# Optimization experiments

Measured on AMD Instinct MI355X. Metric: run time of the kernel, lower is better.

The kernel has to match this reference:

```python
import jax, jax.numpy as jnp
import numpy as np
jax.config.update("jax_enable_x64", True)  # int64 needed for the prime-product duplicate hash

EPSILON = 1e-6
SIGMA_BOOST = 2.0
B, N, CHUNK, R = 16, 4096, 32, 2
K = N // CHUNK            # 128 chunks
GADD, RADD = 8, 8
NPOINTS = 2 ** R + GADD + RADD   # 20 integer tuples per mean
L = CHUNK * NPOINTS              # 640 tuples per chunk
OUT, IN = 1024, 1024
RNG = np.array([OUT, IN], dtype=np.float32)      # subrange for the learned cols (out dim, in dim)
REGION = np.array([8.0, 8.0], dtype=np.float32)  # relative sampling range
# itertools.product([True, False], repeat=2) -> floor/ceil selection mask
FLOOR_MASK = jnp.array([[True, True], [True, False], [False, True], [False, False]])


def setup_inputs() -> dict:
    key = jax.random.key(0)
    ks = jax.random.split(key, 6)
    return {
        "input": jax.random.normal(ks[0], (B, IN), jnp.float32),
        "res": jax.random.normal(ks[1], (B, N, R + 2), jnp.float32),   # raw hypernetwork output
        "bias": jax.random.normal(ks[2], (OUT,), jnp.float32),          # dense bias (Bias.DENSE)
        "u_global": jax.random.uniform(ks[3], (B, K, CHUNK, GADD, R), jnp.float32),
        "u_rel": jax.random.uniform(ks[4], (B, K, CHUNK, RADD, R), jnp.float32),
        "temp_indices": jax.random.randint(ks[5], (N, 2), 0, OUT, jnp.int64),
    }


def reference(input, res, bias, u_global, u_rel, temp_indices):
    rngv = jnp.asarray(RNG)    # (R,) sizes of learned dims
    rrng = jnp.asarray(REGION)

    # ---- split_out: activations on raw hypernetwork output ----
    means = jax.nn.sigmoid(res[:, :, :R]) * (rngv - 1.0)                                  # (B,N,R)
    sigmas = (jax.nn.softplus(res[:, :, R] + SIGMA_BOOST) + EPSILON)[:, :, None] * rngv   # (B,N,R)
    values = res[:, :, R + 1]                                                             # (B,N)

    means = means.reshape(B, K, CHUNK, R)
    sigmas = sigmas.reshape(B, K, CHUNK, R)
    values = values.reshape(B, K, CHUNK)

    # ---- generate_integer_tuples (non-differentiable: uses means.data) ----
    m = jax.lax.stop_gradient(means)
    mexp = m[:, :, :, None, :]                                       # (B,K,C,1,R)
    neighbor = jnp.where(FLOOR_MASK[None, None, None], jnp.floor(mexp), jnp.ceil(mexp))  # (B,K,C,4,R)
    sampled = jnp.floor(u_global * (1.0 - EPSILON) * rngv)           # (B,K,C,GADD,R)
    mns = jnp.round(m)[:, :, :, None, :]
    lower = mns - rrng * 0.5
    upper = mns + rrng * 0.5
    lower = jnp.where(lower < 0.0, 0.0, lower)
    lower = jnp.where(upper > rngv, rngv - rrng, lower)
    rr = jnp.floor(u_rel * (1.0 - EPSILON) * rrng + lower)           # (B,K,C,RADD,R)
    ints = jnp.concatenate([neighbor, sampled, rr], axis=3)          # (B,K,C,NPOINTS,R)
    ints = ints.reshape(B, K, L, R).astype(jnp.int64)

    # ---- duplicates: prime-product hash, sort, compare neighbors, unsort ----
    primes = jnp.array([2, 3], jnp.int64)[:R]
    h = jnp.prod((ints + 1) ** primes, axis=-1)                      # (B,K,L) int64
    sidx = jnp.argsort(h, axis=2)
    hs = jnp.take_along_axis(h, sidx, 2)
    dmask = jnp.concatenate([jnp.zeros((B, K, 1), bool), hs[:, :, 1:] == hs[:, :, :-1]], axis=2)
    dups = jnp.take_along_axis(dmask, jnp.argsort(sidx, axis=2), 2)  # (B,K,L)

    # ---- densities: sum_r (p-m)^2/(eps+sigma), via quadratic expansion (avoids 5D tensor) ----
    pts = ints.astype(jnp.float32)                                   # (B,K,L,R)
    isig = 1.0 / (EPSILON + sigmas)                                  # (B,K,C,R)
    t1 = jnp.einsum('bklr,bkcr->bklc', pts * pts, isig)
    t2 = jnp.einsum('bklr,bkcr->bklc', pts, isig * means)
    t3 = jnp.sum(isig * means * means, axis=-1)                      # (B,K,C)
    props = jnp.exp(-0.5 * (t1 - 2.0 * t2 + t3[:, :, None, :]))      # (B,K,L,C)

    # zero duplicates, normalize over tuples, distribute values
    props = props * (~dups)[:, :, :, None].astype(jnp.float32)
    props = props / jnp.sum(props, axis=2, keepdims=True)
    vals = jnp.sum(props * values[:, :, None, :], axis=3)            # (B,K,L)

    # ---- stitch learned columns into the hardwired template ----
    flat_idx = ints.reshape(B, K * L, R)
    template = jnp.broadcast_to(temp_indices[None, :, None, :], (B, N, NPOINTS, 2)).reshape(B, K * L, 2)
    full_idx = template.at[:, :, jnp.array([0, 1])].set(flat_idx)    # learn_cols = (0, 1)
    out_idx = full_idx[:, :, 0]                                      # index into out_size
    in_idx = full_idx[:, :, 1]                                       # index into input dim
    vflat = vals.reshape(B, K * L)

    # ---- sparse matrix * input: gather, weight, scatter-add ----
    gathered = vflat * jnp.take_along_axis(input, in_idx, axis=1)    # (B, K*L)
    flat = (jnp.arange(B)[:, None] * OUT + out_idx).reshape(-1)
    y = jnp.zeros((B * OUT,), jnp.float32).at[flat].add(gathered.reshape(-1)).reshape(B, OUT)
    return y + bias[None, :]
```

## Files before the change

### kernel.cpp

```cpp
#include <hip/hip_runtime.h>
#include <hip/hip_fp16.h>
#include <math.h>

#define NBATCH 16
#define CH     32
#define NP     20
#define LPTS   640
#define DIMO   1024
#define TAB    2048

__global__ void init_out_kernel(const float* __restrict__ bias, float* __restrict__ out) {
    int i = blockIdx.x * blockDim.x + threadIdx.x;
    if (i < NBATCH * DIMO) out[i] = bias[i & (DIMO - 1)];
}

__device__ __forceinline__ float wave_sum63(float v) {
    v += __int_as_float(__builtin_amdgcn_update_dpp(0, __float_as_int(v), 0x111, 0xF, 0xF, true));
    v += __int_as_float(__builtin_amdgcn_update_dpp(0, __float_as_int(v), 0x112, 0xF, 0xF, true));
    v += __int_as_float(__builtin_amdgcn_update_dpp(0, __float_as_int(v), 0x114, 0xF, 0xF, true));
    v += __int_as_float(__builtin_amdgcn_update_dpp(0, __float_as_int(v), 0x118, 0xF, 0xF, true));
    v += __int_as_float(__builtin_amdgcn_update_dpp(0, __float_as_int(v), 0x142, 0xA, 0xF, true));
    v += __int_as_float(__builtin_amdgcn_update_dpp(0, __float_as_int(v), 0x143, 0xC, 0xF, true));
    return v;
}

__global__ __launch_bounds__(LPTS, 8) void hyper_kernel(
    const float* __restrict__ input,
    const float* __restrict__ res,
    const float* __restrict__ u_global,
    const float* __restrict__ u_rel,
    float* __restrict__ out)
{
    __shared__ float4 cpar[CH];
    __shared__ float cm0[CH], cm1[CH], cval[CH], colsum[CH];
    __shared__ __align__(16) float cscale[CH];
    __shared__ unsigned long long keys[TAB];
    __shared__ int mins[TAB];
    __shared__ float outacc[DIMO];

    const int bk  = blockIdx.x;
    const int b   = bk >> 7;
    const int tid = threadIdx.x;

    #pragma unroll
    for (int i = tid; i < TAB; i += LPTS) { keys[i] = 0ULL; mins[i] = 0x7fffffff; }
    outacc[tid] = 0.0f;
    if (tid < DIMO - LPTS) outacc[tid + LPTS] = 0.0f;

    if (tid < CH) {
        colsum[tid] = 0.0f;
        const float* rp = res + (size_t)(bk * CH + tid) * 4;
        const float r0 = rp[0], r1 = rp[1], r2 = rp[2], r3 = rp[3];
        const float m0 = (1.0f / (1.0f + expf(-r0))) * 1023.0f;
        const float m1 = (1.0f / (1.0f + expf(-r1))) * 1023.0f;
        const float xx = r2 + 2.0f;
        const float sp = fmaxf(xx, 0.0f) + log1pf(expf(-fabsf(xx)));
        const float sig = (sp + 1e-6f) * 1024.0f;
        const float isig = 1.0f / (1e-6f + sig);
        cm0[tid] = m0; cm1[tid] = m1;
        cpar[tid] = make_float4(isig, isig * m0, isig * m1, isig * (m0 * m0 + m1 * m1));
        cval[tid] = r3;
    }
    __syncthreads();

    const int c = tid / NP;
    const int p = tid - c * NP;
    const float m0 = cm0[c], m1 = cm1[c];
    const float CEPS = (float)(1.0 - 1e-6);

    int x, y;
    if (p < 4) {
        x = (int)((p & 2) ? ceilf(m0) : floorf(m0));
        y = (int)((p & 1) ? ceilf(m1) : floorf(m1));
    } else if (p < 12) {
        const float* up = u_global + (size_t)(((bk * CH + c) * 8 + (p - 4)) * 2);
        x = (int)floorf((up[0] * CEPS) * 1024.0f);
        y = (int)floorf((up[1] * CEPS) * 1024.0f);
    } else {
        const float* up = u_rel + (size_t)(((bk * CH + c) * 8 + (p - 12)) * 2);
        const float mn0 = rintf(m0), mn1 = rintf(m1);
        float lo0 = mn0 - 4.0f; if (lo0 < 0.0f) lo0 = 0.0f; if (mn0 + 4.0f > 1024.0f) lo0 = 1016.0f;
        float lo1 = mn1 - 4.0f; if (lo1 < 0.0f) lo1 = 0.0f; if (mn1 + 4.0f > 1024.0f) lo1 = 1016.0f;
        x = (int)floorf((up[0] * CEPS) * 8.0f + lo0);
        y = (int)floorf((up[1] * CEPS) * 8.0f + lo1);
    }

    const long long xi = (long long)x + 1;
    const long long yi = (long long)y + 1;
    const unsigned long long h = (unsigned long long)(xi * xi * (yi * yi * yi));

    unsigned int hh = (unsigned int)(h ^ (h >> 31));
    hh *= 2654435761u;
    int idx = (int)(hh >> 21);
    for (;;) {
        unsigned long long prev = atomicCAS(&keys[idx], 0ULL, h);
        if (prev == 0ULL || prev == h) break;
        idx = (idx + 1) & (TAB - 1);
    }
    atomicMin(&mins[idx], tid);
    __syncthreads();
    const float keep = (mins[idx] == tid) ? 1.0f : 0.0f;

    const float px = (float)x, py = (float)y;
    const float p2 = px * px + py * py;
    const bool lane63 = (tid & 63) == 63;

    __half2 pc[CH / 2];
    #pragma unroll
    for (int j = 0; j < CH / 2; ++j) {
        const float4 cp0 = cpar[2 * j];
        const float4 cp1 = cpar[2 * j + 1];
        const float d0 = cp0.x * p2 - 2.0f * (px * cp0.y + py * cp0.z) + cp0.w;
        const float d1 = cp1.x * p2 - 2.0f * (px * cp1.y + py * cp1.z) + cp1.w;
        const float v0 = __expf(-0.5f * d0) * keep;
        const float v1 = __expf(-0.5f * d1) * keep;
        pc[j] = __floats2half2_rn(v0, v1);
        const float s0 = wave_sum63(v0);
        const float s1 = wave_sum63(v1);
        if (lane63) {
            atomicAdd(&colsum[2 * j], s0);
            atomicAdd(&colsum[2 * j + 1], s1);
        }
    }
    __syncthreads();
    if (tid < CH) cscale[tid] = cval[tid] / colsum[tid];
    __syncthreads();

    float val = 0.0f;
    const float4* cs4 = reinterpret_cast<const float4*>(cscale);
    #pragma unroll
    for (int i = 0; i < CH / 4; ++i) {
        const float4 sc = cs4[i];
        const float2 f0 = __half22float2(pc[2 * i]);
        const float2 f1 = __half22float2(pc[2 * i + 1]);
        val += f0.x * sc.x + f0.y * sc.y + f1.x * sc.z + f1.y * sc.w;
    }

    const float g = val * input[b * DIMO + y];
    atomicAdd(&outacc[x], g);
    __syncthreads();

    {
        const float v0 = outacc[tid];
        if (v0 != 0.0f) atomicAdd(&out[b * DIMO + tid], v0);
        if (tid < DIMO - LPTS) {
            const float v1 = outacc[tid + LPTS];
            if (v1 != 0.0f) atomicAdd(&out[b * DIMO + tid + LPTS], v1);
        }
    }
}

extern "C" void kernel_launch(void* const* d_in, const int* in_sizes, int n_in,
                              void* d_out, int out_size, void* d_ws, size_t ws_size,
                              hipStream_t stream) {
    const float* input  = (const float*)d_in[0];
    const float* res    = (const float*)d_in[1];
    const float* bias   = (const float*)d_in[2];
    const float* u_glob = (const float*)d_in[3];
    const float* u_rel  = (const float*)d_in[4];
    float* out = (float*)d_out;

    hipLaunchKernelGGL(init_out_kernel, dim3((NBATCH * DIMO + 255) / 256), dim3(256), 0, stream,
                       bias, out);
    hipLaunchKernelGGL(hyper_kernel, dim3(NBATCH * 128), dim3(LPTS), 0, stream,
                       input, res, u_glob, u_rel, out);
}
```

Baseline: 125.0 us.

## Process two tuples per thread, alias output accumulator onto hash table, fold bias

Halves the block size to 320 threads, each handling two tuples (chunks c and c+16), so the wave reductions for column sums cover two values at once. The shared outacc buffer reuses the hash-key storage after dedup, which cuts LDS use per block. The init kernel is replaced by a memset, with bias added by the kk==0 block of each batch. Hashing now uses 32-bit products and float2 loads. More registers per thread may limit occupancy.

```diff
diff --git a/kernel.cpp b/kernel.cpp
--- a/kernel.cpp
+++ b/kernel.cpp
@@ -6,13 +6,9 @@
 #define CH     32
 #define NP     20
 #define LPTS   640
+#define NT     320
 #define DIMO   1024
 #define TAB    2048
-
-__global__ void init_out_kernel(const float* __restrict__ bias, float* __restrict__ out) {
-    int i = blockIdx.x * blockDim.x + threadIdx.x;
-    if (i < NBATCH * DIMO) out[i] = bias[i & (DIMO - 1)];
-}
 
 __device__ __forceinline__ float wave_sum63(float v) {
     v += __int_as_float(__builtin_amdgcn_update_dpp(0, __float_as_int(v), 0x111, 0xF, 0xF, true));
@@ -24,9 +20,10 @@
     return v;
 }
 
-__global__ __launch_bounds__(LPTS, 8) void hyper_kernel(
+__global__ __launch_bounds__(NT, 8) void hyper_kernel(
     const float* __restrict__ input,
     const float* __restrict__ res,
+    const float* __restrict__ bias,
     const float* __restrict__ u_global,
     const float* __restrict__ u_rel,
     float* __restrict__ out)
@@ -36,16 +33,17 @@
     __shared__ __align__(16) float cscale[CH];
     __shared__ unsigned long long keys[TAB];
     __shared__ int mins[TAB];
-    __shared__ float outacc[DIMO];
+    float* const outacc = reinterpret_cast<float*>(keys);
 
     const int bk  = blockIdx.x;
     const int b   = bk >> 7;
+    const int kk  = bk & 127;
     const int tid = threadIdx.x;
+    const int c0  = tid / NP;
+    const int p   = tid - c0 * NP;
+    const int c1  = c0 + 16;
 
-    #pragma unroll
-    for (int i = tid; i < TAB; i += LPTS) { keys[i] = 0ULL; mins[i] = 0x7fffffff; }
-    outacc[tid] = 0.0f;
-    if (tid < DIMO - LPTS) outacc[tid + LPTS] = 0.0f;
+    for (int i = tid; i < TAB; i += NT) { keys[i] = 0ULL; mins[i] = 0x7fffffff; }
 
     if (tid < CH) {
         colsum[tid] = 0.0f;
@@ -63,90 +61,119 @@
     }
     __syncthreads();
 
-    const int c = tid / NP;
-    const int p = tid - c * NP;
-    const float m0 = cm0[c], m1 = cm1[c];
     const float CEPS = (float)(1.0 - 1e-6);
-
-    int x, y;
-    if (p < 4) {
-        x = (int)((p & 2) ? ceilf(m0) : floorf(m0));
-        y = (int)((p & 1) ? ceilf(m1) : floorf(m1));
-    } else if (p < 12) {
-        const float* up = u_global + (size_t)(((bk * CH + c) * 8 + (p - 4)) * 2);
-        x = (int)floorf((up[0] * CEPS) * 1024.0f);
-        y = (int)floorf((up[1] * CEPS) * 1024.0f);
-    } else {
-        const float* up = u_rel + (size_t)(((bk * CH + c) * 8 + (p - 12)) * 2);
-        const float mn0 = rintf(m0), mn1 = rintf(m1);
-        float lo0 = mn0 - 4.0f; if (lo0 < 0.0f) lo0 = 0.0f; if (mn0 + 4.0f > 1024.0f) lo0 = 1016.0f;
-        float lo1 = mn1 - 4.0f; if (lo1 < 0.0f) lo1 = 0.0f; if (mn1 + 4.0f > 1024.0f) lo1 = 1016.0f;
-        x = (int)floorf((up[0] * CEPS) * 8.0f + lo0);
-        y = (int)floorf((up[1] * CEPS) * 8.0f + lo1);
+    int x0, y0, x1, y1;
+    {
+        const float2* ug = reinterpret_cast<const float2*>(u_global);
+        const float2* ur = reinterpret_cast<const float2*>(u_rel);
+        #pragma unroll
+        for (int q = 0; q < 2; ++q) {
+            const int c = q ? c1 : c0;
+            const float m0 = cm0[c], m1 = cm1[c];
+            int x, y;
+            if (p < 4) {
+                x = (int)((p & 2) ? ceilf(m0) : floorf(m0));
+                y = (int)((p & 1) ? ceilf(m1) : floorf(m1));
+            } else if (p < 12) {
+                const float2 u = ug[(bk * CH + c) * 8 + (p - 4)];
+                x = (int)floorf((u.x * CEPS) * 1024.0f);
+                y = (int)floorf((u.y * CEPS) * 1024.0f);
+            } else {
+                const float2 u = ur[(bk * CH + c) * 8 + (p - 12)];
+                const float mn0 = rintf(m0), mn1 = rintf(m1);
+                float lo0 = mn0 - 4.0f; if (lo0 < 0.0f) lo0 = 0.0f; if (mn0 + 4.0f > 1024.0f) lo0 = 1016.0f;
+                float lo1 = mn1 - 4.0f; if (lo1 < 0.0f) lo1 = 0.0f; if (mn1 + 4.0f > 1024.0f) lo1 = 1016.0f;
+                x = (int)floorf((u.x * CEPS) * 8.0f + lo0);
+                y = (int)floorf((u.y * CEPS) * 8.0f + lo1);
+            }
+            if (q) { x1 = x; y1 = y; } else { x0 = x; y0 = y; }
+        }
     }
 
-    const long long xi = (long long)x + 1;
-    const long long yi = (long long)y + 1;
-    const unsigned long long h = (unsigned long long)(xi * xi * (yi * yi * yi));
+    const float in0 = input[b * DIMO + y0];
+    const float in1 = input[b * DIMO + y1];
 
-    unsigned int hh = (unsigned int)(h ^ (h >> 31));
-    hh *= 2654435761u;
-    int idx = (int)(hh >> 21);
-    for (;;) {
-        unsigned long long prev = atomicCAS(&keys[idx], 0ULL, h);
-        if (prev == 0ULL || prev == h) break;
-        idx = (idx + 1) & (TAB - 1);
+    int idxA, idxB;
+    {
+        const unsigned int a0 = (unsigned int)((x0 + 1) * (x0 + 1));
+        const unsigned int b3_0 = (unsigned int)((y0 + 1) * (y0 + 1) * (y0 + 1));
+        const unsigned long long h0 = (unsigned long long)a0 * b3_0;
+        const unsigned int a1 = (unsigned int)((x1 + 1) * (x1 + 1));
+        const unsigned int b3_1 = (unsigned int)((y1 + 1) * (y1 + 1) * (y1 + 1));
+        const unsigned long long h1 = (unsigned long long)a1 * b3_1;
+
+        unsigned int hhA = (unsigned int)(h0 ^ (h0 >> 31)) * 2654435761u;
+        idxA = (int)(hhA >> 21);
+        for (;;) {
+            unsigned long long prev = atomicCAS(&keys[idxA], 0ULL, h0);
+            if (prev == 0ULL || prev == h0) break;
+            idxA = (idxA + 1) & (TAB - 1);
+        }
+        atomicMin(&mins[idxA], tid);
+
+        unsigned int hhB = (unsigned int)(h1 ^ (h1 >> 31)) * 2654435761u;
+        idxB = (int)(hhB >> 21);
+        for (;;) {
+            unsigned long long prev = atomicCAS(&keys[idxB], 0ULL, h1);
+            if (prev == 0ULL || prev == h1) break;
+            idxB = (idxB + 1) & (TAB - 1);
+        }
+        atomicMin(&mins[idxB], tid + NT);
     }
-    atomicMin(&mins[idx], tid);
     __syncthreads();
-    const float keep = (mins[idx] == tid) ? 1.0f : 0.0f;
+    const float keep0 = (mins[idxA] == tid)      ? 1.0f : 0.0f;
+    const float keep1 = (mins[idxB] == tid + NT) ? 1.0f : 0.0f;
 
-    const float px = (float)x, py = (float)y;
-    const float p2 = px * px + py * py;
+    for (int i = tid; i < DIMO; i += NT) outacc[i] = (kk == 0) ? bias[i] : 0.0f;
+
+    const float px0 = (float)x0, py0 = (float)y0;
+    const float px1 = (float)x1, py1 = (float)y1;
+    const float p20 = px0 * px0 + py0 * py0;
+    const float p21 = px1 * px1 + py1 * py1;
     const bool lane63 = (tid & 63) == 63;
 
-    __half2 pc[CH / 2];
+    __half2 pc0[CH / 2], pc1[CH / 2];
     #pragma unroll
     for (int j = 0; j < CH / 2; ++j) {
-        const float4 cp0 = cpar[2 * j];
-        const float4 cp1 = cpar[2 * j + 1];
-        const float d0 = cp0.x * p2 - 2.0f * (px * cp0.y + py * cp0.z) + cp0.w;
-        const float d1 = cp1.x * p2 - 2.0f * (px * cp1.y + py * cp1.z) + cp1.w;
-        const float v0 = __expf(-0.5f * d0) * keep;
-        const float v1 = __expf(-0.5f * d1) * keep;
-        pc[j] = __floats2half2_rn(v0, v1);
-        const float s0 = wave_sum63(v0);
-        const float s1 = wave_sum63(v1);
+        const float4 cpA = cpar[2 * j];
+        const float4 cpB = cpar[2 * j + 1];
+        const float vA0 = __expf(-0.5f * (cpA.x * p20 - 2.0f * (px0 * cpA.y + py0 * cpA.z) + cpA.w)) * keep0;
+        const float vB0 = __expf(-0.5f * (cpB.x * p20 - 2.0f * (px0 * cpB.y + py0 * cpB.z) + cpB.w)) * keep0;
+        const float vA1 = __expf(-0.5f * (cpA.x * p21 - 2.0f * (px1 * cpA.y + py1 * cpA.z) + cpA.w)) * keep1;
+        const float vB1 = __expf(-0.5f * (cpB.x * p21 - 2.0f * (px1 * cpB.y + py1 * cpB.z) + cpB.w)) * keep1;
+        pc0[j] = __floats2half2_rn(vA0, vB0);
+        pc1[j] = __floats2half2_rn(vA1, vB1);
+        const float sA = wave_sum63(vA0 + vA1);
+        const float sB = wave_sum63(vB0 + vB1);
         if (lane63) {
-            atomicAdd(&colsum[2 * j], s0);
-            atomicAdd(&colsum[2 * j + 1], s1);
+            atomicAdd(&colsum[2 * j], sA);
+            atomicAdd(&colsum[2 * j + 1], sB);
         }
     }
     __syncthreads();
     if (tid < CH) cscale[tid] = cval[tid] / colsum[tid];
     __syncthreads();
 
-    float val = 0.0f;
+    float val0 = 0.0f, val1 = 0.0f;
     const float4* cs4 = reinterpret_cast<const float4*>(cscale);
     #pragma unroll
     for (int i = 0; i < CH / 4; ++i) {
         const float4 sc = cs4[i];
-        const float2 f0 = __half22float2(pc[2 * i]);
-        const float2 f1 = __half22float2(pc[2 * i + 1]);
-        val += f0.x * sc.x + f0.y * sc.y + f1.x * sc.z + f1.y * sc.w;
+        const float2 a0 = __half22float2(pc0[2 * i]);
+        const float2 b0 = __half22float2(pc0[2 * i + 1]);
+        val0 += a0.x * sc.x + a0.y * sc.y + b0.x * sc.z + b0.y * sc.w;
+        const float2 a1 = __half22float2(pc1[2 * i]);
+        const float2 b1 = __half22float2(pc1[2 * i + 1]);
+        val1 += a1.x * sc.x + a1.y * sc.y + b1.x * sc.z + b1.y * sc.w;
     }
 
-    const float g = val * input[b * DIMO + y];
-    atomicAdd(&outacc[x], g);
+    atomicAdd(&outacc[x0], val0 * in0);
+    atomicAdd(&outacc[x1], val1 * in1);
     __syncthreads();
 
-    {
-        const float v0 = outacc[tid];
-        if (v0 != 0.0f) atomicAdd(&out[b * DIMO + tid], v0);
-        if (tid < DIMO - LPTS) {
-            const float v1 = outacc[tid + LPTS];
-            if (v1 != 0.0f) atomicAdd(&out[b * DIMO + tid + LPTS], v1);
-        }
+    for (int i = tid; i < DIMO; i += NT) {
+        const float v = outacc[i];
+        if (v != 0.0f) atomicAdd(&out[b * DIMO + i], v);
     }
 }
 
@@ -160,8 +187,7 @@
     const float* u_rel  = (const float*)d_in[4];
     float* out = (float*)d_out;
 
-    hipLaunchKernelGGL(init_out_kernel, dim3((NBATCH * DIMO + 255) / 256), dim3(256), 0, stream,
-                       bias, out);
-    hipLaunchKernelGGL(hyper_kernel, dim3(NBATCH * 128), dim3(LPTS), 0, stream,
-                       input, res, u_glob, u_rel, out);
+    hipMemsetAsync(out, 0, (size_t)NBATCH * DIMO * sizeof(float), stream);
+    hipLaunchKernelGGL(hyper_kernel, dim3(NBATCH * 128), dim3(NT), 0, stream,
+                       input, res, bias, u_glob, u_rel, out);
 }
```

Measured after the change: 118.2 us. -5.4%, faster.
